# Kernel tuning notes

Hardware: AMD Instinct MI355X
Metric: run time of the kernel (lower is better)

## Reference

```python
import jax, jax.numpy as jnp
import numpy as np

N = 100_000   # nodes
E = 200_000   # edges
D = 768       # d_model
L = 4         # gnn_layers
AF, AV = 9, 64   # atom feature columns, atom vocab
BF, BV = 3, 8    # bond feature columns, bond vocab


def layer_norm(x, g, b, eps=1e-5):
    m = x.mean(-1, keepdims=True)
    v = x.var(-1, keepdims=True)
    return (x - m) * jax.lax.rsqrt(v + eps) * g + b


def setup_inputs() -> dict:
    key = jax.random.key(0)
    keys = iter(jax.random.split(key, 40))
    w = lambda shape: jax.random.normal(next(keys), shape, jnp.float32) * 0.02
    return {
        "x": jax.random.randint(next(keys), (N, AF), 0, AV),
        "edge_attr": jax.random.randint(next(keys), (E, BF), 0, BV),
        "edge_index": jax.random.randint(next(keys), (2, E), 0, N),
        # AtomEncoder params (9 embedding tables stacked)
        "atom_emb": w((AF, AV, D)),
        "atom_ln_g": jnp.ones((D,)), "atom_ln_b": jnp.zeros((D,)),
        "atom_w1": w((D, D)), "atom_b1": jnp.zeros((D,)),
        "atom_w2": w((D, D)), "atom_b2": jnp.zeros((D,)),
        # BondEncoder params (3 embedding tables stacked)
        "bond_emb": w((BF, BV, D)),
        "bond_ln_g": jnp.ones((D,)), "bond_ln_b": jnp.zeros((D,)),
        "bond_w1": w((D, D)), "bond_b1": jnp.zeros((D,)),
        "bond_w2": w((D, D)), "bond_b2": jnp.zeros((D,)),
        # per-layer GINEConv MLP (Linear-ReLU-Linear) and LayerNorm, stacked on L
        "conv_w1": w((L, D, D)), "conv_b1": jnp.zeros((L, D)),
        "conv_w2": w((L, D, D)), "conv_b2": jnp.zeros((L, D)),
        "ln_g": jnp.ones((L, D)), "ln_b": jnp.zeros((L, D)),
    }


def reference(x, edge_attr, edge_index,
              atom_emb, atom_ln_g, atom_ln_b, atom_w1, atom_b1, atom_w2, atom_b2,
              bond_emb, bond_ln_g, bond_ln_b, bond_w1, bond_b1, bond_w2, bond_b2,
              conv_w1, conv_b1, conv_w2, conv_b2, ln_g, ln_b):
    gelu = lambda t: jax.nn.gelu(t, approximate=False)  # torch default GELU is exact

    # AtomEncoder: sum of per-column embeddings -> LN -> Linear/GELU/Linear
    h = atom_emb[jnp.arange(AF), x].sum(axis=1)            # [N, D]
    h = layer_norm(h, atom_ln_g, atom_ln_b)
    h = gelu(h @ atom_w1 + atom_b1) @ atom_w2 + atom_b2

    # BondEncoder
    e = bond_emb[jnp.arange(BF), edge_attr].sum(axis=1)    # [E, D]
    e = layer_norm(e, bond_ln_g, bond_ln_b)
    e = gelu(e @ bond_w1 + bond_b1) @ bond_w2 + bond_b2

    src, dst = edge_index[0], edge_index[1]
    for l in range(L):
        # GINEConv (eps=0): aggr_i = sum_{j->i} relu(h_j + e_ji); out = mlp(h_i + aggr_i)
        msg = jax.nn.relu(h[src] + e)                      # [E, D] gather + add
        aggr = jax.ops.segment_sum(msg, dst, num_segments=N)
        z = h + aggr
        z = jax.nn.relu(z @ conv_w1[l] + conv_b1[l]) @ conv_w2[l] + conv_b2[l]
        z = gelu(z)                                        # dropout=0 (eval)
        h = layer_norm(z + h, ln_g[l], ln_b[l])
    return h
```

## Files before the change

kernel.cpp:

```cpp
#include <hip/hip_runtime.h>

#define DM 768
#define SCAN_BS 1024

using u16 = unsigned short;
using u32 = unsigned int;

typedef __attribute__((ext_vector_type(8))) __bf16 bf16x8;
typedef __attribute__((ext_vector_type(4))) float f32x4;
typedef __attribute__((address_space(1))) void gvoid;
typedef __attribute__((address_space(3))) void lvoid;

__device__ __forceinline__ float bf2f(u16 h) { return __uint_as_float(((u32)h) << 16); }
__device__ __forceinline__ u16 f2bf(float f) {
    u32 u = __float_as_uint(f);
    u32 r = (u + 0x7FFFu + ((u >> 16) & 1u)) >> 16;
    return (u16)r;
}
__device__ __forceinline__ float gelu_f(float x) {
    float y = 0.7978845608f * x * (1.f + 0.044715f * x * x);
    float e = __expf(2.f * y);
    float th = 1.f - 2.f * __builtin_amdgcn_rcpf(e + 1.f);
    return 0.5f * x * (1.f + th);
}

__global__ __launch_bounds__(256) void prep_weights(
    const float* __restrict__ aw1, const float* __restrict__ aw2,
    const float* __restrict__ bw1, const float* __restrict__ bw2,
    const float* __restrict__ cw1, const float* __restrict__ cw2,
    u16* __restrict__ wbt)
{
    int z = blockIdx.z;
    const float* W;
    if (z == 0) W = aw1;
    else if (z == 1) W = aw2;
    else if (z == 2) W = bw1;
    else if (z == 3) W = bw2;
    else if (z < 8) W = cw1 + (size_t)(z - 4) * DM * DM;
    else W = cw2 + (size_t)(z - 8) * DM * DM;
    u16* out = wbt + (size_t)z * DM * DM;

    __shared__ float tile[32][33];
    int bx = blockIdx.x * 32, by = blockIdx.y * 32;
    int tx = threadIdx.x & 31, ty = threadIdx.x >> 5;
    #pragma unroll
    for (int i = ty; i < 32; i += 8) tile[i][tx] = W[(size_t)(by + i) * DM + bx + tx];
    __syncthreads();
    #pragma unroll
    for (int i = ty; i < 32; i += 8) out[(size_t)(bx + i) * DM + by + tx] = f2bf(tile[tx][i]);
}

__global__ __launch_bounds__(192) void encode_ln9(
    const int* __restrict__ idx,
    const float* __restrict__ emb, const float* __restrict__ g, const float* __restrict__ bb,
    u16* __restrict__ out)
{
    long n = blockIdx.x;
    int t = threadIdx.x;
    int d = t * 4;
    __shared__ int feat[12];
    __shared__ float sred[8];
    if (t < 9) feat[t] = idx[n * 9 + t];
    __syncthreads();
    float a0 = 0.f, a1 = 0.f, a2 = 0.f, a3 = 0.f;
    #pragma unroll
    for (int f = 0; f < 9; f++) {
        const float* rp = emb + (size_t)f * 64 * DM + (size_t)feat[f] * DM + d;
        float4 v = *reinterpret_cast<const float4*>(rp);
        a0 += v.x; a1 += v.y; a2 += v.z; a3 += v.w;
    }
    float s = a0 + a1 + a2 + a3;
    float s2 = a0 * a0 + a1 * a1 + a2 * a2 + a3 * a3;
    #pragma unroll
    for (int o = 32; o; o >>= 1) { s += __shfl_down(s, o); s2 += __shfl_down(s2, o); }
    int wid = t >> 6;
    if ((t & 63) == 0) { sred[wid] = s; sred[4 + wid] = s2; }
    __syncthreads();
    float S = sred[0] + sred[1] + sred[2];
    float S2 = sred[4] + sred[5] + sred[6];
    float mean = S * (1.f / 768.f);
    float var = S2 * (1.f / 768.f) - mean * mean;
    float rstd = rsqrtf(var + 1e-5f);
    ushort4 o;
    o.x = f2bf((a0 - mean) * rstd * g[d + 0] + bb[d + 0]);
    o.y = f2bf((a1 - mean) * rstd * g[d + 1] + bb[d + 1]);
    o.z = f2bf((a2 - mean) * rstd * g[d + 2] + bb[d + 2]);
    o.w = f2bf((a3 - mean) * rstd * g[d + 3] + bb[d + 3]);
    *reinterpret_cast<ushort4*>(out + n * DM + d) = o;
}

__global__ __launch_bounds__(256) void encode_ln_bond(
    const float* __restrict__ emb, const float* __restrict__ g, const float* __restrict__ bb,
    u16* __restrict__ out)
{
    int key = blockIdx.x;
    int t = threadIdx.x;
    __shared__ float sred[16];
    int f0 = key & 7, f1 = (key >> 3) & 7, f2 = (key >> 6) & 7;
    float v[3];
    float s = 0.f, s2 = 0.f;
    #pragma unroll
    for (int j = 0; j < 3; j++) {
        int d = t + j * 256;
        float a = emb[(0 * 8 + f0) * DM + d] + emb[(1 * 8 + f1) * DM + d] + emb[(2 * 8 + f2) * DM + d];
        v[j] = a; s += a; s2 += a * a;
    }
    #pragma unroll
    for (int o = 32; o; o >>= 1) { s += __shfl_down(s, o); s2 += __shfl_down(s2, o); }
    int wid = t >> 6;
    if ((t & 63) == 0) { sred[wid] = s; sred[8 + wid] = s2; }
    __syncthreads();
    if (t == 0) {
        sred[0] = sred[0] + sred[1] + sred[2] + sred[3];
        sred[8] = sred[8] + sred[9] + sred[10] + sred[11];
    }
    __syncthreads();
    float mean = sred[0] * (1.f / 768.f);
    float var = sred[8] * (1.f / 768.f) - mean * mean;
    float rstd = rsqrtf(var + 1e-5f);
    #pragma unroll
    for (int j = 0; j < 3; j++) {
        int d = t + j * 256;
        out[(long)key * DM + d] = f2bf((v[j] - mean) * rstd * g[d] + bb[d]);
    }
}

__global__ __launch_bounds__(192) void layer_ln(
    const u16* __restrict__ y, const u16* __restrict__ holdb,
    const float* __restrict__ g, const float* __restrict__ bb,
    u16* __restrict__ hb, float* __restrict__ dout)
{
    long n = blockIdx.x;
    int t = threadIdx.x;
    int d = t * 4;
    __shared__ float sred[8];
    ushort4 yv = *reinterpret_cast<const ushort4*>(y + n * DM + d);
    ushort4 hv = *reinterpret_cast<const ushort4*>(holdb + n * DM + d);
    float v0 = bf2f(yv.x) + bf2f(hv.x);
    float v1 = bf2f(yv.y) + bf2f(hv.y);
    float v2 = bf2f(yv.z) + bf2f(hv.z);
    float v3 = bf2f(yv.w) + bf2f(hv.w);
    float s = v0 + v1 + v2 + v3;
    float s2 = v0 * v0 + v1 * v1 + v2 * v2 + v3 * v3;
    #pragma unroll
    for (int o = 32; o; o >>= 1) { s += __shfl_down(s, o); s2 += __shfl_down(s2, o); }
    int wid = t >> 6;
    if ((t & 63) == 0) { sred[wid] = s; sred[4 + wid] = s2; }
    __syncthreads();
    float S = sred[0] + sred[1] + sred[2];
    float S2 = sred[4] + sred[5] + sred[6];
    float mean = S * (1.f / 768.f);
    float var = S2 * (1.f / 768.f) - mean * mean;
    float rstd = rsqrtf(var + 1e-5f);
    float r0 = (v0 - mean) * rstd * g[d + 0] + bb[d + 0];
    float r1 = (v1 - mean) * rstd * g[d + 1] + bb[d + 1];
    float r2 = (v2 - mean) * rstd * g[d + 2] + bb[d + 2];
    float r3 = (v3 - mean) * rstd * g[d + 3] + bb[d + 3];
    if (dout) {
        float4 o = { r0, r1, r2, r3 };
        *reinterpret_cast<float4*>(dout + n * DM + d) = o;
    } else {
        ushort4 o;
        o.x = f2bf(r0); o.y = f2bf(r1); o.z = f2bf(r2); o.w = f2bf(r3);
        *reinterpret_cast<ushort4*>(hb + n * DM + d) = o;
    }
}

__global__ __launch_bounds__(256) void csr_count(const int* __restrict__ dst, int* __restrict__ deg, int E)
{
    int e = blockIdx.x * 256 + threadIdx.x;
    if (e < E) atomicAdd(&deg[dst[e]], 1);
}

__global__ __launch_bounds__(SCAN_BS) void scan_block(const int* __restrict__ deg, int* __restrict__ tmp,
                                                      int* __restrict__ bsum, int n)
{
    __shared__ int sh[SCAN_BS];
    int gid = blockIdx.x * SCAN_BS + threadIdx.x;
    int v = (gid < n) ? deg[gid] : 0;
    sh[threadIdx.x] = v;
    __syncthreads();
    for (int o = 1; o < SCAN_BS; o <<= 1) {
        int add = (threadIdx.x >= o) ? sh[threadIdx.x - o] : 0;
        __syncthreads();
        sh[threadIdx.x] += add;
        __syncthreads();
    }
    if (gid < n) tmp[gid] = sh[threadIdx.x];
    if (threadIdx.x == SCAN_BS - 1) bsum[blockIdx.x] = sh[SCAN_BS - 1];
}

__global__ __launch_bounds__(SCAN_BS) void scan_bsum(int* __restrict__ bsum, int nb)
{
    __shared__ int sh[SCAN_BS];
    int v = (threadIdx.x < nb) ? bsum[threadIdx.x] : 0;
    sh[threadIdx.x] = v;
    __syncthreads();
    for (int o = 1; o < SCAN_BS; o <<= 1) {
        int add = (threadIdx.x >= o) ? sh[threadIdx.x - o] : 0;
        __syncthreads();
        sh[threadIdx.x] += add;
        __syncthreads();
    }
    if (threadIdx.x < nb) bsum[threadIdx.x] = sh[threadIdx.x];
}

__global__ __launch_bounds__(256) void scan_final(const int* __restrict__ tmp, const int* __restrict__ bsum,
                                                  const int* __restrict__ deg, int* __restrict__ offs,
                                                  int* __restrict__ cursor, int n)
{
    int gid = blockIdx.x * 256 + threadIdx.x;
    if (gid >= n) return;
    int b = gid / SCAN_BS;
    int inc = tmp[gid] + (b > 0 ? bsum[b - 1] : 0);
    offs[gid + 1] = inc;
    cursor[gid] = inc - deg[gid];
    if (gid == 0) offs[0] = 0;
}

__global__ __launch_bounds__(256) void csr_fill(const int* __restrict__ dst, int* __restrict__ cursor,
                                                int* __restrict__ perm, int E)
{
    int e = blockIdx.x * 256 + threadIdx.x;
    if (e < E) {
        int p = atomicAdd(&cursor[dst[e]], 1);
        perm[p] = e;
    }
}

__global__ __launch_bounds__(256) void pack_edges(
    const int* __restrict__ src, const int* __restrict__ eattr, const int* __restrict__ perm,
    u32* __restrict__ ep, int E)
{
    int k = blockIdx.x * 256 + threadIdx.x;
    if (k < E) {
        int eid = perm[k];
        int key = eattr[eid * 3 + 0] + (eattr[eid * 3 + 1] << 3) + (eattr[eid * 3 + 2] << 6);
        ep[k] = ((u32)src[eid] << 9) | (u32)key;
    }
}

__global__ __launch_bounds__(192) void aggregate(
    const u16* __restrict__ h, const u16* __restrict__ ebtab,
    const u32* __restrict__ ep, const int* __restrict__ offs,
    u16* __restrict__ out)
{
    long n = blockIdx.x;
    int t = threadIdx.x;
    int d = t * 4;
    ushort4 a = *reinterpret_cast<const ushort4*>(h + n * DM + d);
    float acc0 = bf2f(a.x), acc1 = bf2f(a.y), acc2 = bf2f(a.z), acc3 = bf2f(a.w);
    int beg = offs[n], end = offs[n + 1];
    for (int k = beg; k < end; k++) {
        u32 pk = ep[k];
        long s = pk >> 9;
        long key = pk & 511;
        ushort4 hv = *reinterpret_cast<const ushort4*>(h + s * DM + d);
        ushort4 ev = *reinterpret_cast<const ushort4*>(ebtab + key * DM + d);
        acc0 += fmaxf(0.f, bf2f(hv.x) + bf2f(ev.x));
        acc1 += fmaxf(0.f, bf2f(hv.y) + bf2f(ev.y));
        acc2 += fmaxf(0.f, bf2f(hv.z) + bf2f(ev.z));
        acc3 += fmaxf(0.f, bf2f(hv.w) + bf2f(ev.w));
    }
    ushort4 o;
    o.x = f2bf(acc0); o.y = f2bf(acc1); o.z = f2bf(acc2); o.w = f2bf(acc3);
    *reinterpret_cast<ushort4*>(out + n * DM + d) = o;
}

union GemmSmem {
    u16 tiles[3][2][128 * 32];
    u16 ctile[128 * 136];
};

template <int ACT>
__global__ __launch_bounds__(256) void gemm128(
    const u16* __restrict__ A, const u16* __restrict__ Bt,
    const float* __restrict__ bias, u16* __restrict__ outB)
{
    __shared__ GemmSmem sm;
    const int tid = threadIdx.x;
    const int lane = tid & 63, wid = tid >> 6;
    const int wr = wid >> 1, wc = wid & 1;

    const int nwg = gridDim.x;
    const int orig = blockIdx.x;
    const int q8 = nwg >> 3, r8 = nwg & 7;
    const int xcd = orig & 7, idx8 = orig >> 3;
    const int w = (xcd < r8 ? xcd * (q8 + 1) : r8 * (q8 + 1) + (xcd - r8) * q8) + idx8;
    const int n0 = (w % 6) * 128;
    const long m0 = (long)(w / 6) * 128;

    f32x4 acc[4][4] = {};

    const int ch0 = tid, ch1 = 256 + tid;
    const int r0_ = ch0 >> 2, k0_ = (ch0 & 3) ^ ((r0_ >> 1) & 3);
    const int r1_ = ch1 >> 2, k1_ = (ch1 & 3) ^ ((r1_ >> 1) & 3);
    const u16* Ag0 = A + (m0 + r0_) * DM + k0_ * 8;
    const u16* Ag1 = A + (m0 + r1_) * DM + k1_ * 8;
    const u16* Bg0 = Bt + (long)(n0 + r0_) * DM + k0_ * 8;
    const u16* Bg1 = Bt + (long)(n0 + r1_) * DM + k1_ * 8;
    const int lds0 = ((wid << 6)) * 8;
    const int lds1 = (256 + (wid << 6)) * 8;

    auto stage = [&](int buf, int kt) {
        int ko = kt * 32;
        __builtin_amdgcn_global_load_lds((gvoid*)(Ag0 + ko), (lvoid*)&sm.tiles[buf][0][lds0], 16, 0, 0);
        __builtin_amdgcn_global_load_lds((gvoid*)(Ag1 + ko), (lvoid*)&sm.tiles[buf][0][lds1], 16, 0, 0);
        __builtin_amdgcn_global_load_lds((gvoid*)(Bg0 + ko), (lvoid*)&sm.tiles[buf][1][lds0], 16, 0, 0);
        __builtin_amdgcn_global_load_lds((gvoid*)(Bg1 + ko), (lvoid*)&sm.tiles[buf][1][lds1], 16, 0, 0);
    };

    stage(0, 0);
    stage(1, 1);
    asm volatile("s_waitcnt vmcnt(4) lgkmcnt(0)\n\ts_barrier" ::: "memory");

    const int ar = lane & 15, kb = lane >> 4;
    const int kbe = kb ^ ((ar >> 1) & 3);
    const int NT = DM / 32;
    #pragma unroll
    for (int kt = 0; kt < NT; ++kt) {
        const int buf = kt % 3;
        if (kt + 2 < NT) stage((kt + 2) % 3, kt + 2);
        bf16x8 af[4], bv[4];
        #pragma unroll
        for (int m = 0; m < 4; m++)
            af[m] = *reinterpret_cast<const bf16x8*>(&sm.tiles[buf][0][(wr * 64 + m * 16 + ar) * 32 + kbe * 8]);
        #pragma unroll
        for (int n = 0; n < 4; n++)
            bv[n] = *reinterpret_cast<const bf16x8*>(&sm.tiles[buf][1][(wc * 64 + n * 16 + ar) * 32 + kbe * 8]);
        #pragma unroll
        for (int m = 0; m < 4; m++)
            #pragma unroll
            for (int n = 0; n < 4; n++)
                acc[m][n] = __builtin_amdgcn_mfma_f32_16x16x32_bf16(af[m], bv[n], acc[m][n], 0, 0, 0);
        if (kt < NT - 2) {
            asm volatile("s_waitcnt vmcnt(4) lgkmcnt(0)\n\ts_barrier" ::: "memory");
        } else if (kt == NT - 2) {
            asm volatile("s_waitcnt vmcnt(0) lgkmcnt(0)\n\ts_barrier" ::: "memory");
        }
    }
    __syncthreads();

    const int rg4 = (lane >> 4) * 4;
    #pragma unroll
    for (int n = 0; n < 4; n++) {
        int lc = wc * 64 + n * 16 + ar;
        float bvp = bias[n0 + lc];
        #pragma unroll
        for (int m = 0; m < 4; m++) {
            int lr = wr * 64 + m * 16 + rg4;
            #pragma unroll
            for (int j = 0; j < 4; j++) {
                float v = acc[m][n][j] + bvp;
                if (ACT == 1) v = fmaxf(v, 0.f);
                if (ACT == 2) v = gelu_f(v);
                sm.ctile[(lr + j) * 136 + lc] = f2bf(v);
            }
        }
    }
    __syncthreads();
    const int row = tid >> 2, b4 = tid & 3;
    #pragma unroll
    for (int ps = 0; ps < 2; ps++) {
        int rr = row + ps * 64;
        const u16* srcp = &sm.ctile[rr * 136];
        u16* dstp = outB + (m0 + rr) * DM + n0;
        #pragma unroll
        for (int i = 0; i < 4; i++) {
            int c = b4 * 8 + i * 32;
            *reinterpret_cast<uint4*>(dstp + c) = *reinterpret_cast<const uint4*>(srcp + c);
        }
    }
}

extern "C" void kernel_launch(void* const* d_in, const int* in_sizes, int n_in,
                              void* d_out, int out_size, void* d_ws, size_t ws_size,
                              hipStream_t stream)
{
    const int N = in_sizes[0] / 9;
    const int E = in_sizes[1] / 3;
    const int L = 4;
    const long Mpad = ((N + 127) / 128) * 128;
    const int Mtiles = (int)(Mpad / 128);

    const int* x = (const int*)d_in[0];
    const int* eattr = (const int*)d_in[1];
    const int* eidx = (const int*)d_in[2];
    const float* atom_emb = (const float*)d_in[3];
    const float* atom_g = (const float*)d_in[4];
    const float* atom_bb = (const float*)d_in[5];
    const float* atom_w1 = (const float*)d_in[6];
    const float* atom_b1 = (const float*)d_in[7];
    const float* atom_w2 = (const float*)d_in[8];
    const float* atom_b2 = (const float*)d_in[9];
    const float* bond_emb = (const float*)d_in[10];
    const float* bond_g = (const float*)d_in[11];
    const float* bond_bb = (const float*)d_in[12];
    const float* bond_w1 = (const float*)d_in[13];
    const float* bond_b1 = (const float*)d_in[14];
    const float* bond_w2 = (const float*)d_in[15];
    const float* bond_b2 = (const float*)d_in[16];
    const float* conv_w1 = (const float*)d_in[17];
    const float* conv_b1 = (const float*)d_in[18];
    const float* conv_w2 = (const float*)d_in[19];
    const float* conv_b2 = (const float*)d_in[20];
    const float* ln_g = (const float*)d_in[21];
    const float* ln_b = (const float*)d_in[22];
    const int* src = eidx;
    const int* dst = eidx + E;
    float* dout = (float*)d_out;

    char* p = (char*)d_ws;
    auto alloc = [&](size_t bytes) { void* r = (void*)p; p += (bytes + 255) & ~(size_t)255; return r; };
    u16* B2   = (u16*)alloc((size_t)2 * Mpad * DM * 2);
    u16* h_b  = (u16*)alloc((size_t)Mpad * DM * 2);
    u16* wbt  = (u16*)alloc((size_t)12 * DM * DM * 2);
    u16* bt0  = (u16*)alloc((size_t)512 * DM * 2);
    u16* bt1  = (u16*)alloc((size_t)512 * DM * 2);
    u16* ebtab= (u16*)alloc((size_t)512 * DM * 2);
    int* deg    = (int*)alloc((size_t)N * 4);
    int* tmp    = (int*)alloc((size_t)N * 4);
    int* cursor = (int*)alloc((size_t)N * 4);
    int* offs   = (int*)alloc((size_t)(N + 1) * 4);
    int* bsum   = (int*)alloc((size_t)SCAN_BS * 4);
    int* perm   = (int*)alloc((size_t)E * 4);
    u32* ep     = (u32*)alloc((size_t)E * 4);
    u16* B2a = B2;
    u16* B2b = B2 + (size_t)Mpad * DM;

    hipMemsetAsync(deg, 0, (size_t)N * 4, stream);
    csr_count<<<(E + 255) / 256, 256, 0, stream>>>(dst, deg, E);
    const int nb = (N + SCAN_BS - 1) / SCAN_BS;
    scan_block<<<nb, SCAN_BS, 0, stream>>>(deg, tmp, bsum, N);
    scan_bsum<<<1, SCAN_BS, 0, stream>>>(bsum, nb);
    scan_final<<<(N + 255) / 256, 256, 0, stream>>>(tmp, bsum, deg, offs, cursor, N);
    csr_fill<<<(E + 255) / 256, 256, 0, stream>>>(dst, cursor, perm, E);
    pack_edges<<<(E + 255) / 256, 256, 0, stream>>>(src, eattr, perm, ep, E);

    prep_weights<<<dim3(24, 24, 12), 256, 0, stream>>>(atom_w1, atom_w2, bond_w1, bond_w2, conv_w1, conv_w2, wbt);

    encode_ln_bond<<<512, 256, 0, stream>>>(bond_emb, bond_g, bond_bb, bt0);
    gemm128<2><<<6 * 4, 256, 0, stream>>>(bt0, wbt + (size_t)2 * DM * DM, bond_b1, bt1);
    gemm128<0><<<6 * 4, 256, 0, stream>>>(bt1, wbt + (size_t)3 * DM * DM, bond_b2, ebtab);

    encode_ln9<<<N, 192, 0, stream>>>(x, atom_emb, atom_g, atom_bb, B2a);
    gemm128<2><<<6 * Mtiles, 256, 0, stream>>>(B2a, wbt + (size_t)0 * DM * DM, atom_b1, B2b);
    gemm128<0><<<6 * Mtiles, 256, 0, stream>>>(B2b, wbt + (size_t)1 * DM * DM, atom_b2, h_b);

    for (int l = 0; l < L; l++) {
        aggregate<<<N, 192, 0, stream>>>(h_b, ebtab, ep, offs, B2a);
        gemm128<1><<<6 * Mtiles, 256, 0, stream>>>(B2a, wbt + (size_t)(4 + l) * DM * DM, conv_b1 + l * DM, B2b);
        gemm128<2><<<6 * Mtiles, 256, 0, stream>>>(B2b, wbt + (size_t)(8 + l) * DM * DM, conv_b2 + l * DM, B2a);
        layer_ln<<<N, 192, 0, stream>>>(B2a, h_b, ln_g + l * DM, ln_b + l * DM,
                                        h_b, (l == L - 1) ? dout : nullptr);
    }
}
```

Baseline: 2.672 ms.

## Load GEMM B operand directly into registers, stage only A through LDS

The 128x128 GEMM no longer stages the weight (B) tile through LDS. Each wave now loads its B fragments straight from global memory into registers, one k-step ahead, while A keeps the triple-buffered global_load_lds path. This halves LDS traffic and staging, but each wave pair now reads B redundantly from global or L2 memory and uses more registers. The vmcnt waits are adjusted to account for the extra outstanding register loads.

```diff
diff --git a/kernel.cpp b/kernel.cpp
--- a/kernel.cpp
+++ b/kernel.cpp
@@ -268,7 +268,7 @@
 }
 
 union GemmSmem {
-    u16 tiles[3][2][128 * 32];
+    u16 tiles[3][128 * 32];
     u16 ctile[128 * 136];
 };
 
@@ -292,51 +292,64 @@
 
     f32x4 acc[4][4] = {};
 
-    const int ch0 = tid, ch1 = 256 + tid;
-    const int r0_ = ch0 >> 2, k0_ = (ch0 & 3) ^ ((r0_ >> 1) & 3);
-    const int r1_ = ch1 >> 2, k1_ = (ch1 & 3) ^ ((r1_ >> 1) & 3);
+    const int r0_ = tid >> 2, k0_ = (tid & 3) ^ ((r0_ >> 1) & 3);
+    const int c1 = 256 + tid;
+    const int r1_ = c1 >> 2, k1_ = (c1 & 3) ^ ((r1_ >> 1) & 3);
     const u16* Ag0 = A + (m0 + r0_) * DM + k0_ * 8;
     const u16* Ag1 = A + (m0 + r1_) * DM + k1_ * 8;
-    const u16* Bg0 = Bt + (long)(n0 + r0_) * DM + k0_ * 8;
-    const u16* Bg1 = Bt + (long)(n0 + r1_) * DM + k1_ * 8;
-    const int lds0 = ((wid << 6)) * 8;
+    const int lds0 = (wid << 6) * 8;
     const int lds1 = (256 + (wid << 6)) * 8;
 
-    auto stage = [&](int buf, int kt) {
+    auto stageA = [&](int buf, int kt) {
         int ko = kt * 32;
-        __builtin_amdgcn_global_load_lds((gvoid*)(Ag0 + ko), (lvoid*)&sm.tiles[buf][0][lds0], 16, 0, 0);
-        __builtin_amdgcn_global_load_lds((gvoid*)(Ag1 + ko), (lvoid*)&sm.tiles[buf][0][lds1], 16, 0, 0);
-        __builtin_amdgcn_global_load_lds((gvoid*)(Bg0 + ko), (lvoid*)&sm.tiles[buf][1][lds0], 16, 0, 0);
-        __builtin_amdgcn_global_load_lds((gvoid*)(Bg1 + ko), (lvoid*)&sm.tiles[buf][1][lds1], 16, 0, 0);
+        __builtin_amdgcn_global_load_lds((gvoid*)(Ag0 + ko), (lvoid*)&sm.tiles[buf][lds0], 16, 0, 0);
+        __builtin_amdgcn_global_load_lds((gvoid*)(Ag1 + ko), (lvoid*)&sm.tiles[buf][lds1], 16, 0, 0);
     };
-
-    stage(0, 0);
-    stage(1, 1);
-    asm volatile("s_waitcnt vmcnt(4) lgkmcnt(0)\n\ts_barrier" ::: "memory");
 
     const int ar = lane & 15, kb = lane >> 4;
     const int kbe = kb ^ ((ar >> 1) & 3);
+
+    const u16* Brow[4];
+    #pragma unroll
+    for (int n = 0; n < 4; n++)
+        Brow[n] = Bt + (long)(n0 + wc * 64 + n * 16 + ar) * DM + kb * 8;
+
+    bf16x8 bcur[4], bnxt[4];
+
+    stageA(0, 0);
+    stageA(1, 1);
+    asm volatile("" ::: "memory");
+    #pragma unroll
+    for (int n = 0; n < 4; n++)
+        bcur[n] = *reinterpret_cast<const bf16x8*>(Brow[n]);
+    asm volatile("s_waitcnt vmcnt(6) lgkmcnt(0)\n\ts_barrier" ::: "memory");
+
     const int NT = DM / 32;
     #pragma unroll
     for (int kt = 0; kt < NT; ++kt) {
         const int buf = kt % 3;
-        if (kt + 2 < NT) stage((kt + 2) % 3, kt + 2);
-        bf16x8 af[4], bv[4];
+        if (kt + 2 < NT) stageA((kt + 2) % 3, kt + 2);
+        asm volatile("" ::: "memory");
+        if (kt + 1 < NT) {
+            #pragma unroll
+            for (int n = 0; n < 4; n++)
+                bnxt[n] = *reinterpret_cast<const bf16x8*>(Brow[n] + (kt + 1) * 32);
+        }
+        bf16x8 af[4];
         #pragma unroll
         for (int m = 0; m < 4; m++)
-            af[m] = *reinterpret_cast<const bf16x8*>(&sm.tiles[buf][0][(wr * 64 + m * 16 + ar) * 32 + kbe * 8]);
-        #pragma unroll
-        for (int n = 0; n < 4; n++)
-            bv[n] = *reinterpret_cast<const bf16x8*>(&sm.tiles[buf][1][(wc * 64 + n * 16 + ar) * 32 + kbe * 8]);
+            af[m] = *reinterpret_cast<const bf16x8*>(&sm.tiles[buf][(wr * 64 + m * 16 + ar) * 32 + kbe * 8]);
         #pragma unroll
         for (int m = 0; m < 4; m++)
             #pragma unroll
             for (int n = 0; n < 4; n++)
-                acc[m][n] = __builtin_amdgcn_mfma_f32_16x16x32_bf16(af[m], bv[n], acc[m][n], 0, 0, 0);
+                acc[m][n] = __builtin_amdgcn_mfma_f32_16x16x32_bf16(af[m], bcur[n], acc[m][n], 0, 0, 0);
+        #pragma unroll
+        for (int n = 0; n < 4; n++) bcur[n] = bnxt[n];
         if (kt < NT - 2) {
+            asm volatile("s_waitcnt vmcnt(6) lgkmcnt(0)\n\ts_barrier" ::: "memory");
+        } else if (kt == NT - 2) {
             asm volatile("s_waitcnt vmcnt(4) lgkmcnt(0)\n\ts_barrier" ::: "memory");
-        } else if (kt == NT - 2) {
-            asm volatile("s_waitcnt vmcnt(0) lgkmcnt(0)\n\ts_barrier" ::: "memory");
         }
     }
     __syncthreads();
```

New measurement: 3.709 ms. 38.8% more time.
